# Kernel tuning notes

Measured on AMD Instinct MI355X. Metric: run time of the kernel, lower is better.

## Reference

```python
import jax, jax.numpy as jnp
import numpy as np

N, NS, C = 100000, 16, 64
S = 8  # share_planes
EPS = 1e-5

def bn(x, g, b, m, v):
    # eval-mode BatchNorm1d over channel (last) axis
    return (x - m) * (g / jnp.sqrt(v + EPS)) + b

def setup_inputs() -> dict:
    key = jax.random.key(0)
    ks = jax.random.split(key, 24)
    d = {}
    d['p'] = jax.random.normal(ks[0], (N, 3), jnp.float32)
    d['x'] = jax.random.normal(ks[1], (N, C), jnp.float32)
    d['idx'] = jax.random.randint(ks[2], (N, NS), 0, N, jnp.int64)
    d['Wq'] = jax.random.normal(ks[3], (C, C), jnp.float32) * 0.1
    d['bq'] = jax.random.normal(ks[4], (C,), jnp.float32) * 0.1
    d['Wk'] = jax.random.normal(ks[5], (C, C), jnp.float32) * 0.1
    d['bk'] = jax.random.normal(ks[6], (C,), jnp.float32) * 0.1
    d['Wv'] = jax.random.normal(ks[7], (C, C), jnp.float32) * 0.1
    d['bv'] = jax.random.normal(ks[8], (C,), jnp.float32) * 0.1
    d['p_w1'] = jax.random.normal(ks[9], (3, 3), jnp.float32) * 0.5
    d['p_b1'] = jax.random.normal(ks[10], (3,), jnp.float32) * 0.1
    d['p_bn_g'] = jax.random.normal(ks[11], (3,), jnp.float32)
    d['p_bn_b'] = jax.random.normal(ks[12], (3,), jnp.float32) * 0.1
    d['p_bn_m'] = jnp.zeros((3,), jnp.float32)
    d['p_bn_v'] = jnp.ones((3,), jnp.float32)
    d['p_w2'] = jax.random.normal(ks[13], (C, 3), jnp.float32) * 0.3
    d['p_b2'] = jax.random.normal(ks[14], (C,), jnp.float32) * 0.1
    d['w_bn1_g'] = jax.random.normal(ks[15], (C,), jnp.float32)
    d['w_bn1_b'] = jax.random.normal(ks[16], (C,), jnp.float32) * 0.1
    d['w_bn1_m'] = jnp.zeros((C,), jnp.float32)
    d['w_bn1_v'] = jnp.ones((C,), jnp.float32)
    d['w_w1'] = jax.random.normal(ks[17], (C // S, C), jnp.float32) * 0.1
    d['w_b1'] = jax.random.normal(ks[18], (C // S,), jnp.float32) * 0.1
    d['w_bn2_g'] = jax.random.normal(ks[19], (C // S,), jnp.float32)
    d['w_bn2_b'] = jax.random.normal(ks[20], (C // S,), jnp.float32) * 0.1
    d['w_bn2_m'] = jnp.zeros((C // S,), jnp.float32)
    d['w_bn2_v'] = jnp.ones((C // S,), jnp.float32)
    d['w_w2'] = jax.random.normal(ks[21], (C // S, C // S), jnp.float32) * 0.3
    d['w_b2'] = jax.random.normal(ks[22], (C // S,), jnp.float32) * 0.1
    return d

def reference(p, x, idx, Wq, bq, Wk, bk, Wv, bv,
              p_w1, p_b1, p_bn_g, p_bn_b, p_bn_m, p_bn_v, p_w2, p_b2,
              w_bn1_g, w_bn1_b, w_bn1_m, w_bn1_v, w_w1, w_b1,
              w_bn2_g, w_bn2_b, w_bn2_m, w_bn2_v, w_w2, w_b2):
    n, ns = idx.shape
    c = Wv.shape[0]
    s = S
    # q/k/v projections
    x_q = x @ Wq.T + bq                       # (n, c)
    x_k = (x @ Wk.T + bk)[idx]                # (n, ns, c) gather
    x_v = (x @ Wv.T + bv)[idx]                # (n, ns, c) gather
    # relative positions of boundary-KNN neighbors
    p_r = p[idx] - p[:, None, :]              # (n, ns, 3)
    # linear_p: Linear(3,3) -> BN(3) -> ReLU -> Linear(3,c)
    p_r = p_r @ p_w1.T + p_b1
    p_r = jax.nn.relu(bn(p_r, p_bn_g, p_bn_b, p_bn_m, p_bn_v))
    p_r = p_r @ p_w2.T + p_b2                 # (n, ns, c)
    # attention logits (out_planes // mid_planes == 1, so sum(2) is identity)
    w = x_k - x_q[:, None, :] + p_r
    # linear_w: BN(c) -> ReLU -> Linear(c, c/s) -> BN(c/s) -> ReLU -> Linear(c/s, c/s)
    w = jax.nn.relu(bn(w, w_bn1_g, w_bn1_b, w_bn1_m, w_bn1_v))
    w = w @ w_w1.T + w_b1                     # (n, ns, c/s)
    w = jax.nn.relu(bn(w, w_bn2_g, w_bn2_b, w_bn2_m, w_bn2_v))
    w = w @ w_w2.T + w_b2                     # (n, ns, c/s)
    w = jax.nn.softmax(w, axis=1)             # softmax over neighbors
    # grouped weighted reduce with shared attention weights
    out = ((x_v + p_r).reshape(n, ns, s, c // s) * w[:, :, None, :]).sum(1)
    return out.reshape(n, c)
```

## Files before the change

### kernel.cpp

```cpp
#include <hip/hip_runtime.h>
#include <hip/hip_bf16.h>

typedef unsigned short u16;
typedef unsigned int   u32;
typedef __attribute__((ext_vector_type(8))) short bf16x8;
typedef __attribute__((ext_vector_type(4))) float f32x4;

#define EPSV 1e-5f

__device__ __forceinline__ float b2f(u16 u) {
    union { u32 i; float f; } x; x.i = ((u32)u) << 16; return x.f;
}
__device__ __forceinline__ u16 f2b(float f) {
    union { float f; u32 i; } x; x.f = f;
    u32 lsb = (x.i >> 16) & 1u;
    return (u16)((x.i + 0x7fffu + lsb) >> 16);
}
__device__ __forceinline__ bf16x8 pack8(float4 a, float4 b) {
    bf16x8 r;
    r[0] = (short)f2b(a.x); r[1] = (short)f2b(a.y);
    r[2] = (short)f2b(a.z); r[3] = (short)f2b(a.w);
    r[4] = (short)f2b(b.x); r[5] = (short)f2b(b.y);
    r[6] = (short)f2b(b.z); r[7] = (short)f2b(b.w);
    return r;
}

__global__ __launch_bounds__(256) void kvq_mfma(
    const float* __restrict__ x,
    const float* __restrict__ Wq, const float* __restrict__ bq,
    const float* __restrict__ Wk, const float* __restrict__ bk,
    const float* __restrict__ Wv, const float* __restrict__ bv,
    u16* __restrict__ qb, u32* __restrict__ kvb,
    int N)
{
    __shared__ u16 Wl[3 * 64 * 72];
    __shared__ u16 xl[64 * 72];
    const int t = threadIdx.x;

    const float* Wg[3] = {Wq, Wk, Wv};
#pragma unroll
    for (int mat = 0; mat < 3; ++mat) {
        const float4* Wsrc = (const float4*)Wg[mat];
#pragma unroll
        for (int it = 0; it < 4; ++it) {
            int id4 = t + it * 256;
            int row = id4 >> 4;
            int c4  = id4 & 15;
            float4 f = Wsrc[id4];
            u32 lo = (u32)f2b(f.x) | ((u32)f2b(f.y) << 16);
            u32 hi = (u32)f2b(f.z) | ((u32)f2b(f.w) << 16);
            u32* d = (u32*)&Wl[(mat * 64 + row) * 72 + c4 * 4];
            d[0] = lo; d[1] = hi;
        }
    }
    int base = blockIdx.x * 64;
#pragma unroll
    for (int it = 0; it < 4; ++it) {
        int id4 = t + it * 256;
        int row = id4 >> 4;
        int c4  = id4 & 15;
        int gi = base + row; if (gi >= N) gi = N - 1;
        float4 f = ((const float4*)(x + (size_t)gi * 64))[c4];
        u32 lo = (u32)f2b(f.x) | ((u32)f2b(f.y) << 16);
        u32 hi = (u32)f2b(f.z) | ((u32)f2b(f.w) << 16);
        u32* d = (u32*)&xl[row * 72 + c4 * 4];
        d[0] = lo; d[1] = hi;
    }
    __syncthreads();

    const int lane = t & 63;
    const int wid  = t >> 6;
    const int n_   = lane & 15;
    const int quad = lane >> 4;

    bf16x8 a0 = *(const bf16x8*)&xl[(wid * 16 + n_) * 72 + quad * 8];
    bf16x8 a1 = *(const bf16x8*)&xl[(wid * 16 + n_) * 72 + 32 + quad * 8];

    f32x4 acc[12];
#pragma unroll
    for (int nt = 0; nt < 12; ++nt) {
        int mat = nt >> 2;
        int c = ((nt & 3) << 4) + n_;
        bf16x8 b0 = *(const bf16x8*)&Wl[(mat * 64 + c) * 72 + quad * 8];
        bf16x8 b1 = *(const bf16x8*)&Wl[(mat * 64 + c) * 72 + 32 + quad * 8];
        f32x4 z = {0.f, 0.f, 0.f, 0.f};
        z = __builtin_amdgcn_mfma_f32_16x16x32_bf16(a0, b0, z, 0, 0, 0);
        z = __builtin_amdgcn_mfma_f32_16x16x32_bf16(a1, b1, z, 0, 0, 0);
        acc[nt] = z;
    }

    int rbase = base + wid * 16 + quad * 4;
#pragma unroll
    for (int g4 = 0; g4 < 4; ++g4) {
        int c = (g4 << 4) + n_;
        float biasq = bq[c], biask = bk[c], biasv = bv[c];
#pragma unroll
        for (int r = 0; r < 4; ++r) {
            int i2 = rbase + r;
            if (i2 < N) {
                qb[(size_t)i2 * 64 + c] = f2b(acc[g4][r] + biasq);
                u32 kvp = (u32)f2b(acc[4 + g4][r] + biask)
                        | ((u32)f2b(acc[8 + g4][r] + biasv) << 16);
                kvb[(size_t)i2 * 64 + c] = kvp;
            }
        }
    }
}

__global__ __launch_bounds__(256) void attn_mfma(
    const float* __restrict__ p, const int* __restrict__ idx32,
    const u16* __restrict__ qb, const u32* __restrict__ kvb,
    const float* __restrict__ pw1, const float* __restrict__ pb1,
    const float* __restrict__ g3, const float* __restrict__ b3,
    const float* __restrict__ m3, const float* __restrict__ v3,
    const float* __restrict__ pw2, const float* __restrict__ pb2,
    const float* __restrict__ g1, const float* __restrict__ b1,
    const float* __restrict__ m1, const float* __restrict__ v1,
    const float* __restrict__ ww1, const float* __restrict__ wb1,
    const float* __restrict__ g2, const float* __restrict__ b2c,
    const float* __restrict__ m2, const float* __restrict__ v2,
    const float* __restrict__ ww2, const float* __restrict__ wb2,
    float* __restrict__ out, int N)
{
    __shared__ u16   wrT[4][16 * 72];
    __shared__ u16   hbnT[4][16 * 16];
    __shared__ float wT[4][16 * 9];

    const int lane = threadIdx.x & 63;
    const int wid  = threadIdx.x >> 6;
    int i = blockIdx.x * 4 + wid;
    bool active = (i < N);
    int ic = active ? i : 0;
    const int m    = lane & 7;
    const int n16  = lane & 15;
    const int quad = lane >> 4;

    bool idx64 = (idx32[1] == 0) & (idx32[3] == 0) & (idx32[5] == 0) & (idx32[7] == 0);

    float qc  = b2f(qb[(size_t)ic * 64 + lane]);
    float s1  = g1[lane] * rsqrtf(v1[lane] + EPSV);
    float bb1 = b1[lane] - m1[lane] * s1;
    float pw2_0 = pw2[lane * 3 + 0];
    float pw2_1 = pw2[lane * 3 + 1];
    float pw2_2 = pw2[lane * 3 + 2];
    float pb2c  = pb2[lane];
    float s2   = g2[m] * rsqrtf(v2[m] + EPSV);
    float bb2v = b2c[m] - m2[m] * s2;
    float wb1m = wb1[m];
    float wb2m = wb2[m];
    float pix = p[(size_t)ic * 3 + 0];
    float piy = p[(size_t)ic * 3 + 1];
    float piz = p[(size_t)ic * 3 + 2];

    size_t ii = (size_t)ic * 16 + n16;
    int nbr = idx64 ? idx32[ii * 2] : idx32[ii];
    if ((unsigned)nbr >= (unsigned)N) nbr = 0;

    float u0l, u1l, u2l;
    {
        float pdx = p[(size_t)nbr * 3 + 0] - pix;
        float pdy = p[(size_t)nbr * 3 + 1] - piy;
        float pdz = p[(size_t)nbr * 3 + 2] - piz;
        float a0 = pw1[0] * pdx + pw1[1] * pdy + pw1[2] * pdz + pb1[0];
        float a1 = pw1[3] * pdx + pw1[4] * pdy + pw1[5] * pdz + pb1[1];
        float a2 = pw1[6] * pdx + pw1[7] * pdy + pw1[8] * pdz + pb1[2];
        float sa0 = g3[0] * rsqrtf(v3[0] + EPSV);
        float sa1 = g3[1] * rsqrtf(v3[1] + EPSV);
        float sa2 = g3[2] * rsqrtf(v3[2] + EPSV);
        u0l = fmaxf(0.f, a0 * sa0 + (b3[0] - m3[0] * sa0));
        u1l = fmaxf(0.f, a1 * sa1 + (b3[1] - m3[1] * sa1));
        u2l = fmaxf(0.f, a2 * sa2 + (b3[2] - m3[2] * sa2));
    }

    bf16x8 b0, b1f;
    {
        const float4* r4 = (const float4*)(ww1 + (size_t)m * 64);
        b0  = pack8(r4[quad * 2 + 0], r4[quad * 2 + 1]);
        b1f = pack8(r4[8 + quad * 2 + 0], r4[8 + quad * 2 + 1]);
    }
    bf16x8 b2f_ = {};
    if (quad == 0) {
        const float4* r4 = (const float4*)(ww2 + (size_t)m * 8);
        b2f_ = pack8(r4[0], r4[1]);
    }

    float vpr[16];
    u16* myWr = wrT[wid];
#pragma unroll
    for (int j = 0; j < 16; ++j) {
        int nj   = __shfl(nbr, j, 64);
        float u0 = __shfl(u0l, j, 64);
        float u1 = __shfl(u1l, j, 64);
        float u2 = __shfl(u2l, j, 64);
        float pr = u0 * pw2_0 + u1 * pw2_1 + u2 * pw2_2 + pb2c;
        u32 w = kvb[(size_t)nj * 64 + lane];
        float kc = b2f((u16)(w & 0xffff));
        float vc = b2f((u16)(w >> 16));
        vpr[j] = vc + pr;
        float wr = fmaxf(0.f, (kc - qc + pr) * s1 + bb1);
        myWr[j * 72 + lane] = f2b(wr);
    }
    __syncthreads();

    bf16x8 a0 = *(const bf16x8*)&myWr[n16 * 72 + quad * 8];
    bf16x8 a1 = *(const bf16x8*)&myWr[n16 * 72 + 32 + quad * 8];
    f32x4 h1 = {0.f, 0.f, 0.f, 0.f};
    h1 = __builtin_amdgcn_mfma_f32_16x16x32_bf16(a0, b0,  h1, 0, 0, 0);
    h1 = __builtin_amdgcn_mfma_f32_16x16x32_bf16(a1, b1f, h1, 0, 0, 0);

    u16* myH = hbnT[wid];
#pragma unroll
    for (int r = 0; r < 4; ++r) {
        float hb = fmaxf(0.f, (h1[r] + wb1m) * s2 + bb2v);
        myH[(quad * 4 + r) * 16 + m] = f2b(hb);
    }
    __syncthreads();

    bf16x8 a2 = {};
    if (quad == 0) a2 = *(const bf16x8*)&myH[n16 * 16];
    f32x4 scd = {0.f, 0.f, 0.f, 0.f};
    scd = __builtin_amdgcn_mfma_f32_16x16x32_bf16(a2, b2f_, scd, 0, 0, 0);

    float e[4];
    float mx = -1e30f;
#pragma unroll
    for (int r = 0; r < 4; ++r) { e[r] = scd[r] + wb2m; mx = fmaxf(mx, e[r]); }
    mx = fmaxf(mx, __shfl_xor(mx, 16, 64));
    mx = fmaxf(mx, __shfl_xor(mx, 32, 64));
    float s = 0.f;
#pragma unroll
    for (int r = 0; r < 4; ++r) { e[r] = __expf(e[r] - mx); s += e[r]; }
    s += __shfl_xor(s, 16, 64);
    s += __shfl_xor(s, 32, 64);
    float rs = 1.f / s;
    float* myW = wT[wid];
#pragma unroll
    for (int r = 0; r < 4; ++r) myW[(quad * 4 + r) * 9 + m] = e[r] * rs;
    __syncthreads();

    float acc = 0.f;
#pragma unroll
    for (int j = 0; j < 16; ++j) acc += myW[j * 9 + m] * vpr[j];
    if (active) out[(size_t)i * 64 + lane] = acc;
}

__global__ __launch_bounds__(256) void attn_fallback(
    const float* __restrict__ p, const int* __restrict__ idx32,
    const float* __restrict__ x,
    const float* __restrict__ Wq, const float* __restrict__ bq,
    const float* __restrict__ Wk, const float* __restrict__ bk,
    const float* __restrict__ Wv, const float* __restrict__ bv,
    const float* __restrict__ pw1, const float* __restrict__ pb1,
    const float* __restrict__ g3, const float* __restrict__ b3,
    const float* __restrict__ m3, const float* __restrict__ v3,
    const float* __restrict__ pw2, const float* __restrict__ pb2,
    const float* __restrict__ g1, const float* __restrict__ b1,
    const float* __restrict__ m1, const float* __restrict__ v1,
    const float* __restrict__ ww1, const float* __restrict__ wb1,
    const float* __restrict__ g2, const float* __restrict__ b2c,
    const float* __restrict__ m2, const float* __restrict__ v2,
    const float* __restrict__ ww2, const float* __restrict__ wb2,
    float* __restrict__ out, int N)
{
    const int lane = threadIdx.x & 63;
    const int wid  = threadIdx.x >> 6;
    int i = blockIdx.x * 4 + wid;
    bool active = (i < N);
    int ic = active ? i : 0;
    const int m = lane & 7;
    const int g = lane >> 3;
    bool idx64 = (idx32[1] == 0) & (idx32[3] == 0) & (idx32[5] == 0) & (idx32[7] == 0);

    float xi = x[(size_t)ic * 64 + lane];
    float qc = bq[lane];
#pragma unroll
    for (int kk = 0; kk < 64; ++kk)
        qc += __shfl(xi, kk, 64) * Wq[(size_t)lane * 64 + kk];
    float wkr[64], wvr[64];
#pragma unroll
    for (int tt = 0; tt < 64; ++tt) {
        wkr[tt] = Wk[(size_t)lane * 64 + tt];
        wvr[tt] = Wv[(size_t)lane * 64 + tt];
    }
    float bkc = bk[lane], bvc = bv[lane];
    float s1  = g1[lane] * rsqrtf(v1[lane] + EPSV);
    float bb1 = b1[lane] - m1[lane] * s1;
    float pw2_0 = pw2[lane * 3 + 0], pw2_1 = pw2[lane * 3 + 1], pw2_2 = pw2[lane * 3 + 2];
    float pb2c  = pb2[lane];
    float w1s[8];
#pragma unroll
    for (int tt = 0; tt < 8; ++tt) w1s[tt] = ww1[m * 64 + g * 8 + tt];
    float w2s[8];
#pragma unroll
    for (int tt = 0; tt < 8; ++tt) w2s[tt] = ww2[m * 8 + tt];
    float wb1m = wb1[m];
    float s2   = g2[m] * rsqrtf(v2[m] + EPSV);
    float bb2  = b2c[m] - m2[m] * s2;
    float wb2m = wb2[m];
    float pix = p[(size_t)ic * 3 + 0], piy = p[(size_t)ic * 3 + 1], piz = p[(size_t)ic * 3 + 2];
    size_t ii = (size_t)ic * 16 + (lane & 15);
    int nbr = idx64 ? idx32[ii * 2] : idx32[ii];
    if ((unsigned)nbr >= (unsigned)N) nbr = 0;
    float u0l, u1l, u2l;
    {
        float pdx = p[(size_t)nbr * 3 + 0] - pix;
        float pdy = p[(size_t)nbr * 3 + 1] - piy;
        float pdz = p[(size_t)nbr * 3 + 2] - piz;
        float a0 = pw1[0] * pdx + pw1[1] * pdy + pw1[2] * pdz + pb1[0];
        float a1 = pw1[3] * pdx + pw1[4] * pdy + pw1[5] * pdz + pb1[1];
        float a2 = pw1[6] * pdx + pw1[7] * pdy + pw1[8] * pdz + pb1[2];
        float sa0 = g3[0] * rsqrtf(v3[0] + EPSV);
        float sa1 = g3[1] * rsqrtf(v3[1] + EPSV);
        float sa2 = g3[2] * rsqrtf(v3[2] + EPSV);
        u0l = fmaxf(0.f, a0 * sa0 + (b3[0] - m3[0] * sa0));
        u1l = fmaxf(0.f, a1 * sa1 + (b3[1] - m3[1] * sa1));
        u2l = fmaxf(0.f, a2 * sa2 + (b3[2] - m3[2] * sa2));
    }
    float sc[16], vpr[16];
#pragma unroll
    for (int j = 0; j < 16; ++j) {
        int nj = __shfl(nbr, j, 64);
        float u0 = __shfl(u0l, j, 64);
        float u1 = __shfl(u1l, j, 64);
        float u2 = __shfl(u2l, j, 64);
        float pr = u0 * pw2_0 + u1 * pw2_1 + u2 * pw2_2 + pb2c;
        float xn = x[(size_t)nj * 64 + lane];
        float kc = bkc, vc = bvc;
#pragma unroll
        for (int kk = 0; kk < 64; ++kk) {
            float xk = __shfl(xn, kk, 64);
            kc += xk * wkr[kk];
            vc += xk * wvr[kk];
        }
        vpr[j] = vc + pr;
        float wr = fmaxf(0.f, (kc - qc + pr) * s1 + bb1);
        float partial = 0.f;
#pragma unroll
        for (int tt = 0; tt < 8; ++tt)
            partial += __shfl(wr, g * 8 + tt, 64) * w1s[tt];
        partial += __shfl_xor(partial, 8, 64);
        partial += __shfl_xor(partial, 16, 64);
        partial += __shfl_xor(partial, 32, 64);
        float hbn = fmaxf(0.f, (partial + wb1m) * s2 + bb2);
        float h2 = wb2m;
#pragma unroll
        for (int mm = 0; mm < 8; ++mm)
            h2 += __shfl(hbn, (lane & 56) | mm, 64) * w2s[mm];
        sc[j] = h2;
    }
    float mx = sc[0];
#pragma unroll
    for (int j = 1; j < 16; ++j) mx = fmaxf(mx, sc[j]);
    float sum = 0.f, acc = 0.f;
#pragma unroll
    for (int j = 0; j < 16; ++j) {
        float e = __expf(sc[j] - mx);
        sum += e;
        acc += e * vpr[j];
    }
    if (active) out[(size_t)i * 64 + lane] = acc / sum;
}

extern "C" void kernel_launch(void* const* d_in, const int* in_sizes, int n_in,
                              void* d_out, int out_size, void* d_ws, size_t ws_size,
                              hipStream_t stream) {
    const float* p   = (const float*)d_in[0];
    const float* x   = (const float*)d_in[1];
    const int* idx   = (const int*)d_in[2];
    const float* Wq  = (const float*)d_in[3];
    const float* bq  = (const float*)d_in[4];
    const float* Wk  = (const float*)d_in[5];
    const float* bk  = (const float*)d_in[6];
    const float* Wv  = (const float*)d_in[7];
    const float* bv  = (const float*)d_in[8];
    const float* pw1 = (const float*)d_in[9];
    const float* pb1 = (const float*)d_in[10];
    const float* g3  = (const float*)d_in[11];
    const float* b3  = (const float*)d_in[12];
    const float* m3  = (const float*)d_in[13];
    const float* v3  = (const float*)d_in[14];
    const float* pw2 = (const float*)d_in[15];
    const float* pb2 = (const float*)d_in[16];
    const float* g1  = (const float*)d_in[17];
    const float* b1  = (const float*)d_in[18];
    const float* m1  = (const float*)d_in[19];
    const float* v1  = (const float*)d_in[20];
    const float* ww1 = (const float*)d_in[21];
    const float* wb1 = (const float*)d_in[22];
    const float* g2  = (const float*)d_in[23];
    const float* b2  = (const float*)d_in[24];
    const float* m2  = (const float*)d_in[25];
    const float* v2  = (const float*)d_in[26];
    const float* ww2 = (const float*)d_in[27];
    const float* wb2 = (const float*)d_in[28];

    int N = in_sizes[0] / 3;
    size_t plane = (size_t)N * 64;
    bool tier1 = ws_size >= plane * 2 + plane * 4;

    u16* qb  = (u16*)d_ws;
    u32* kvb = (u32*)(qb + plane);

    int blocks = (N + 3) / 4;
    float* out = (float*)d_out;

    if (tier1) {
        int gblocks = (N + 63) / 64;
        kvq_mfma<<<gblocks, 256, 0, stream>>>(x, Wq, bq, Wk, bk, Wv, bv, qb, kvb, N);
        attn_mfma<<<blocks, 256, 0, stream>>>(p, idx, qb, kvb,
            pw1, pb1, g3, b3, m3, v3, pw2, pb2, g1, b1, m1, v1, ww1, wb1,
            g2, b2, m2, v2, ww2, wb2, out, N);
    } else {
        attn_fallback<<<blocks, 256, 0, stream>>>(p, idx, x, Wq, bq, Wk, bk, Wv, bv,
            pw1, pb1, g3, b3, m3, v3, pw2, pb2, g1, b1, m1, v1, ww1, wb1,
            g2, b2, m2, v2, ww2, wb2, out, N);
    }
}
```

Baseline: 261.6 us.

## Batch neighbor KV gathers, use readlane broadcasts, replace block barriers with wave-local waits

Issues all 16 neighbor KV gathers up front so their latencies overlap. Replaces shuffle broadcasts with scalar readlane and unpacks the bf16 pair with plain bit ops. Because each wave uses only its own LDS scratch, the block-wide __syncthreads calls become an LDS waitcnt plus a scheduling barrier, which removes cross-wave stalls. The cost is more registers held live and a reliance on lockstep wave execution for LDS visibility.

```diff
diff --git a/kernel.cpp b/kernel.cpp
--- a/kernel.cpp
+++ b/kernel.cpp
@@ -23,6 +23,9 @@
     r[4] = (short)f2b(b.x); r[5] = (short)f2b(b.y);
     r[6] = (short)f2b(b.z); r[7] = (short)f2b(b.w);
     return r;
+}
+__device__ __forceinline__ float rdlane_f(float v, int lane) {
+    return __uint_as_float(__builtin_amdgcn_readlane(__float_as_uint(v), lane));
 }
 
 __global__ __launch_bounds__(256) void kvq_mfma(
@@ -184,23 +187,30 @@
         b2f_ = pack8(r4[0], r4[1]);
     }
 
+    u32 kvw[16];
+#pragma unroll
+    for (int j = 0; j < 16; ++j) {
+        int nj = __builtin_amdgcn_readlane(nbr, j);
+        kvw[j] = kvb[(size_t)nj * 64 + lane];
+    }
+
     float vpr[16];
     u16* myWr = wrT[wid];
 #pragma unroll
     for (int j = 0; j < 16; ++j) {
-        int nj   = __shfl(nbr, j, 64);
-        float u0 = __shfl(u0l, j, 64);
-        float u1 = __shfl(u1l, j, 64);
-        float u2 = __shfl(u2l, j, 64);
-        float pr = u0 * pw2_0 + u1 * pw2_1 + u2 * pw2_2 + pb2c;
-        u32 w = kvb[(size_t)nj * 64 + lane];
-        float kc = b2f((u16)(w & 0xffff));
-        float vc = b2f((u16)(w >> 16));
+        float u0 = rdlane_f(u0l, j);
+        float u1 = rdlane_f(u1l, j);
+        float u2 = rdlane_f(u2l, j);
+        float pr = fmaf(u0, pw2_0, fmaf(u1, pw2_1, fmaf(u2, pw2_2, pb2c)));
+        u32 w = kvw[j];
+        float kc = __uint_as_float(w << 16);
+        float vc = __uint_as_float(w & 0xffff0000u);
         vpr[j] = vc + pr;
         float wr = fmaxf(0.f, (kc - qc + pr) * s1 + bb1);
         myWr[j * 72 + lane] = f2b(wr);
     }
-    __syncthreads();
+    asm volatile("s_waitcnt lgkmcnt(0)" ::: "memory");
+    __builtin_amdgcn_sched_barrier(0);
 
     bf16x8 a0 = *(const bf16x8*)&myWr[n16 * 72 + quad * 8];
     bf16x8 a1 = *(const bf16x8*)&myWr[n16 * 72 + 32 + quad * 8];
@@ -214,7 +224,8 @@
         float hb = fmaxf(0.f, (h1[r] + wb1m) * s2 + bb2v);
         myH[(quad * 4 + r) * 16 + m] = f2b(hb);
     }
-    __syncthreads();
+    asm volatile("s_waitcnt lgkmcnt(0)" ::: "memory");
+    __builtin_amdgcn_sched_barrier(0);
 
     bf16x8 a2 = {};
     if (quad == 0) a2 = *(const bf16x8*)&myH[n16 * 16];
@@ -236,7 +247,8 @@
     float* myW = wT[wid];
 #pragma unroll
     for (int r = 0; r < 4; ++r) myW[(quad * 4 + r) * 9 + m] = e[r] * rs;
-    __syncthreads();
+    asm volatile("s_waitcnt lgkmcnt(0)" ::: "memory");
+    __builtin_amdgcn_sched_barrier(0);
 
     float acc = 0.f;
 #pragma unroll
```

Result: faster. 240.0 us (-8.2%).
